# Performance work log

Hardware: AMD Instinct MI355X
Metric: run time of the kernel (lower is better)

## Reference

```python
import jax, jax.numpy as jnp
import numpy as np

B, S, D = 2, 1024, 4096
HQ, HKV, HD = 32, 8, 128
GROUPS = HQ // HKV          # 4
SCALE = HD ** -0.5


def _rope_tables(key):
    # standard RoPE cos/sin tables, non-interleaved (half-split) layout
    inv_freq = 1.0 / (10000.0 ** (jnp.arange(0, HD, 2, dtype=jnp.float32) / HD))  # [HD/2]
    pos = jnp.arange(S, dtype=jnp.float32)                                        # [S]
    freqs = pos[:, None] * inv_freq[None, :]                                      # [S, HD/2]
    emb = jnp.concatenate([freqs, freqs], axis=-1)                                # [S, HD]
    cos = jnp.broadcast_to(jnp.cos(emb)[None], (B, S, HD))
    sin = jnp.broadcast_to(jnp.sin(emb)[None], (B, S, HD))
    return cos, sin


def setup_inputs() -> dict:
    key = jax.random.key(0)
    ks = jax.random.split(key, 6)
    hidden_states = jax.random.normal(ks[0], (B, S, D), dtype=jnp.float32)
    cos_table, sin_table = _rope_tables(ks[1])
    Wq = jax.random.normal(ks[2], (D, HQ * HD), dtype=jnp.float32) * (D ** -0.5)
    Wk = jax.random.normal(ks[3], (D, HKV * HD), dtype=jnp.float32) * (D ** -0.5)
    Wv = jax.random.normal(ks[4], (D, HKV * HD), dtype=jnp.float32) * (D ** -0.5)
    Wo = jax.random.normal(ks[5], (HQ * HD, D), dtype=jnp.float32) * ((HQ * HD) ** -0.5)
    return {"hidden_states": hidden_states, "cos_table": cos_table,
            "sin_table": sin_table, "Wq": Wq, "Wk": Wk, "Wv": Wv, "Wo": Wo}


def _rotate_half(x):
    x1, x2 = jnp.split(x, 2, axis=-1)
    return jnp.concatenate([-x2, x1], axis=-1)


def _apply_rope(x, cos, sin):
    # x: [B, S, H, HD]; cos/sin: [B, S, HD] broadcast across heads
    c = cos[:, :, None, :]
    s = sin[:, :, None, :]
    return x * c + _rotate_half(x) * s


def reference(hidden_states, cos_table, sin_table, Wq, Wk, Wv, Wo):
    b, s, _ = hidden_states.shape
    # QKV projections (no bias, Llama-style)
    q = (hidden_states @ Wq).reshape(b, s, HQ, HD)
    k = (hidden_states @ Wk).reshape(b, s, HKV, HD)
    v = (hidden_states @ Wv).reshape(b, s, HKV, HD)
    # fused RoPE on q and k (in [B, S, H, HD] layout, as in source)
    q = _apply_rope(q, cos_table, sin_table)
    k = _apply_rope(k, cos_table, sin_table)
    # -> [B, H, S, HD]
    q = q.transpose(0, 2, 1, 3)
    k = k.transpose(0, 2, 1, 3)
    v = v.transpose(0, 2, 1, 3)
    # GQA repeat_kv: [B, HKV, S, HD] -> [B, HQ, S, HD]
    k = jnp.repeat(k, GROUPS, axis=1)
    v = jnp.repeat(v, GROUPS, axis=1)
    # SDPA, no mask (source calls sdpa without a mask)
    scores = jnp.einsum('bhqd,bhkd->bhqk', q, k) * SCALE
    attn = jax.nn.softmax(scores, axis=-1)
    out = jnp.einsum('bhqk,bhkd->bhqd', attn, v)
    out = out.transpose(0, 2, 1, 3).reshape(b, s, HQ * HD)
    return out @ Wo
```

## Files before the change

kernel.cpp:

```cpp
#include <hip/hip_runtime.h>

#define B_   2
#define S_   1024
#define D_   4096
#define HQ_  32
#define HKV_ 8
#define HD_  128
#define SCALE_ 0.08838834764831845f

typedef unsigned short u16;
typedef __attribute__((ext_vector_type(8))) short s16x8;
typedef __attribute__((ext_vector_type(4))) short s16x4;
typedef __attribute__((ext_vector_type(4))) float f32x4;

#define MFMA(a,b,c) __builtin_amdgcn_mfma_f32_16x16x32_bf16((a),(b),(c),0,0,0)

__device__ __forceinline__ u16 bf16_rne(float x) {
  unsigned u = __float_as_uint(x);
  u += 0x7fffu + ((u >> 16) & 1u);
  return (u16)(u >> 16);
}
__device__ __forceinline__ float bf16_up(u16 h) {
  return __uint_as_float(((unsigned)h) << 16);
}
__device__ __forceinline__ void split2(float x, u16& h, u16& l) {
  h = bf16_rne(x);
  l = bf16_rne(x - bf16_up(h));
}

__device__ __forceinline__ void cvt_hi_lo(float a, float b, unsigned& hi, unsigned& lo) {
  unsigned h, l;
  asm("v_cvt_pk_bf16_f32 %0, %1, %2" : "=v"(h) : "v"(a), "v"(b));
  float ra = __uint_as_float(h << 16);
  float rb = __uint_as_float(h & 0xffff0000u);
  float la = a - ra, lb = b - rb;
  asm("v_cvt_pk_bf16_f32 %0, %1, %2" : "=v"(l) : "v"(la), "v"(lb));
  hi = h; lo = l;
}
__device__ __forceinline__ void pack8(float4 x, float4 y, uint4& h, uint4& l) {
  unsigned h0,h1,h2,h3,l0,l1,l2,l3;
  cvt_hi_lo(x.x, x.y, h0, l0);
  cvt_hi_lo(x.z, x.w, h1, l1);
  cvt_hi_lo(y.x, y.y, h2, l2);
  cvt_hi_lo(y.z, y.w, h3, l3);
  h = make_uint4(h0,h1,h2,h3); l = make_uint4(l0,l1,l2,l3);
}

typedef const __attribute__((address_space(1))) void* gas_ptr;
typedef __attribute__((address_space(3))) void* las_ptr;
__device__ __forceinline__ void gload_lds16(const void* g, void* l) {
  __builtin_amdgcn_global_load_lds((gas_ptr)g, (las_ptr)l, 16, 0, 0);
}

__global__ __launch_bounds__(256) void frag_b2(
    const float* __restrict__ W, u16* __restrict__ dh, u16* __restrict__ dl,
    int N, int n0, int Ntot16, int ntoff)
{
  __shared__ float T[32][68];
  const int kt = blockIdx.x, nbk = blockIdx.y;
  const int tid = threadIdx.x;
#pragma unroll
  for (int rep = 0; rep < 2; ++rep) {
    int idx = tid + rep * 256;
    int row = idx >> 4, c4 = (idx & 15) * 4;
    float4 v = *reinterpret_cast<const float4*>(&W[(size_t)(kt*32 + row) * N + n0 + nbk*64 + c4]);
    *reinterpret_cast<float4*>(&T[row][c4]) = v;
  }
  __syncthreads();
  int c = tid;
  int nt = c >> 6, l = c & 63;
  const size_t base = (((size_t)(kt >> 1) * Ntot16 + ntoff + nbk*4 + nt) * 2 + (kt & 1)) * 512;
  u16 hh[8], ll[8];
#pragma unroll
  for (int j = 0; j < 8; ++j) split2(T[(l >> 4)*8 + j][nt*16 + (l & 15)], hh[j], ll[j]);
  *reinterpret_cast<s16x8*>(&dh[base + (size_t)l * 8]) =
    (s16x8){(short)hh[0],(short)hh[1],(short)hh[2],(short)hh[3],
            (short)hh[4],(short)hh[5],(short)hh[6],(short)hh[7]};
  *reinterpret_cast<s16x8*>(&dl[base + (size_t)l * 8]) =
    (s16x8){(short)ll[0],(short)ll[1],(short)ll[2],(short)ll[3],
            (short)ll[4],(short)ll[5],(short)ll[6],(short)ll[7]};
}

__global__ __launch_bounds__(256) void frag_a(
    const float* __restrict__ src, u16* __restrict__ dh, u16* __restrict__ dl)
{
  __shared__ float T[128][68];
  const int kt = blockIdx.x;
  const int mb = blockIdx.y;
  const int tid = threadIdx.x;
#pragma unroll
  for (int rep = 0; rep < 8; ++rep) {
    int idx = tid + rep * 256;
    int row = idx >> 4, c4 = (idx & 15) * 4;
    float4 v = *reinterpret_cast<const float4*>(&src[(size_t)(mb*128 + row) * 4096 + kt*64 + c4]);
    *reinterpret_cast<float4*>(&T[row][c4]) = v;
  }
  __syncthreads();
#pragma unroll
  for (int rep = 0; rep < 4; ++rep) {
    int c = tid + rep * 256;
    int mt = c >> 7, rem = c & 127, kk = rem >> 6, l = rem & 63;
    u16 hh[8], ll[8];
#pragma unroll
    for (int j = 0; j < 8; ++j)
      split2(T[mt*16 + (l & 15)][kk*32 + (l >> 4)*8 + j], hh[j], ll[j]);
    size_t off = (((size_t)(kt*128 + mb*8 + mt)) * 2 + kk) * 512 + (size_t)l * 8;
    *reinterpret_cast<s16x8*>(&dh[off]) =
      (s16x8){(short)hh[0],(short)hh[1],(short)hh[2],(short)hh[3],
              (short)hh[4],(short)hh[5],(short)hh[6],(short)hh[7]};
    *reinterpret_cast<s16x8*>(&dl[off]) =
      (s16x8){(short)ll[0],(short)ll[1],(short)ll[2],(short)ll[3],
              (short)ll[4],(short)ll[5],(short)ll[6],(short)ll[7]};
  }
}

template<int NF, bool RQ>
__device__ __forceinline__ void gemm256_core(
    const u16* __restrict__ PAh, const u16* __restrict__ PAl,
    const u16* __restrict__ PBh, const u16* __restrict__ PBl,
    float* __restrict__ C0, float* __restrict__ C1, float* __restrict__ C2,
    int ldc0, int Nt16, int mb, int nb, int k0, int nk, u16* L)
{
  const int tid  = threadIdx.x;
  const int lane = tid & 63;
  const int wid  = tid >> 6;
  const int loff = lane * 8;
  const int wm8  = (wid >> 2) * 8;
  const int wnf  = (wid & 3) * NF;

  u16* A0 = L;
  u16* A1 = L + 16384;
  u16* B0 = L + 32768;
  u16* B1 = L + 32768 + NF*4096;

  f32x4 acc[8][NF];
#pragma unroll
  for (int i = 0; i < 8; ++i)
#pragma unroll
    for (int j = 0; j < NF; ++j) acc[i][j] = (f32x4){0.f,0.f,0.f,0.f};

  auto STAGE = [&](int t, u16* la_, u16* lb_) {
    const int kt64 = t >> 1, kk = t & 1;
    const size_t aSlab = (size_t)kt64 * 131072;
    const size_t bSlab = (size_t)kt64 * ((size_t)Nt16 * 1024);
    const int NCH = 32 + 8*NF;
#pragma unroll
    for (int c = wid; c < NCH; c += 8) {
      const u16* src; u16* dst;
      if (c < 16) {
        src = PAh + aSlab + (((size_t)(mb*16 + c))*2 + kk)*512;
        dst = la_ + c*512;
      } else if (c < 32) {
        int m = c - 16;
        src = PAl + aSlab + (((size_t)(mb*16 + m))*2 + kk)*512;
        dst = la_ + 8192 + m*512;
      } else if (c < 32 + 4*NF) {
        int n = c - 32;
        src = PBh + bSlab + (((size_t)(nb*4*NF + n))*2 + kk)*512;
        dst = lb_ + n*512;
      } else {
        int n = c - 32 - 4*NF;
        src = PBl + bSlab + (((size_t)(nb*4*NF + n))*2 + kk)*512;
        dst = lb_ + NF*2048 + n*512;
      }
      gload_lds16(src + loff, dst);
    }
  };

  STAGE(k0, (k0 & 1) ? A1 : A0, (k0 & 1) ? B1 : B0);
  __syncthreads();

  for (int t = k0; t < k0 + nk; ++t) {
    u16* la = (t & 1) ? A1 : A0;
    u16* lb = (t & 1) ? B1 : B0;
    if (t + 1 < k0 + nk)
      STAGE(t + 1, (t & 1) ? A0 : A1, (t & 1) ? B0 : B1);

    s16x8 ah[8], al[8], bh[NF], bl[NF];
#pragma unroll
    for (int mf = 0; mf < 8; ++mf)
      ah[mf] = *reinterpret_cast<const s16x8*>(&la[(wm8+mf)*512 + loff]);
#pragma unroll
    for (int nf = 0; nf < NF; ++nf)
      bh[nf] = *reinterpret_cast<const s16x8*>(&lb[(wnf+nf)*512 + loff]);
    __builtin_amdgcn_s_setprio(1);
#pragma unroll
    for (int nf = 0; nf < NF; ++nf)
#pragma unroll
      for (int mf = 0; mf < 8; ++mf)
        acc[mf][nf] = MFMA(ah[mf], bh[nf], acc[mf][nf]);
    __builtin_amdgcn_s_setprio(0);
#pragma unroll
    for (int mf = 0; mf < 8; ++mf)
      al[mf] = *reinterpret_cast<const s16x8*>(&la[8192 + (wm8+mf)*512 + loff]);
    __builtin_amdgcn_s_setprio(1);
#pragma unroll
    for (int nf = 0; nf < NF; ++nf)
#pragma unroll
      for (int mf = 0; mf < 8; ++mf)
        acc[mf][nf] = MFMA(al[mf], bh[nf], acc[mf][nf]);
    __builtin_amdgcn_s_setprio(0);
#pragma unroll
    for (int nf = 0; nf < NF; ++nf)
      bl[nf] = *reinterpret_cast<const s16x8*>(&lb[NF*2048 + (wnf+nf)*512 + loff]);
    __builtin_amdgcn_s_setprio(1);
#pragma unroll
    for (int nf = 0; nf < NF; ++nf)
#pragma unroll
      for (int mf = 0; mf < 8; ++mf)
        acc[mf][nf] = MFMA(ah[mf], bl[nf], acc[mf][nf]);
    __builtin_amdgcn_s_setprio(0);
    __syncthreads();
  }

  const int lg = lane >> 4, lr = lane & 15;
  const int rowb = mb*256 + (wid >> 2) * 128;
#pragma unroll
  for (int mf = 0; mf < 8; ++mf)
#pragma unroll
    for (int nf = 0; nf < NF; ++nf)
#pragma unroll
      for (int r = 0; r < 4; ++r) {
        int row = rowb + mf*16 + lg*4 + r;
        float v = acc[mf][nf][r];
        if constexpr (RQ) {
          int gcol = nb*(NF*64) + (wid & 3)*(NF*16) + nf*16 + lr;
          if (gcol < 4096)      C0[(size_t)row * 4096 + gcol] = v;
          else if (gcol < 5120) C1[(size_t)row * 1024 + (gcol - 4096)] = v;
          else                  C2[(size_t)row * 1024 + (gcol - 5120)] = v;
        } else {
          int col = nb*(NF*64) + (wid & 3)*(NF*16) + nf*16 + lr;
          C0[(size_t)row * ldc0 + col] = v;
        }
      }
}

__global__ __launch_bounds__(512) void gemm_qkv3(
    const u16* __restrict__ XAh, const u16* __restrict__ XAl,
    const u16* __restrict__ WBh, const u16* __restrict__ WBl,
    float* __restrict__ qb, float* __restrict__ kb, float* __restrict__ vb)
{
  __shared__ __attribute__((aligned(16))) u16 L[57344];
  int id = blockIdx.x;
  int swz = (id & 7) * 32 + (id >> 3);
  int mb = swz >> 5, nb = swz & 31;
  gemm256_core<3, true>(XAh, XAl, WBh, WBl, qb, kb, vb, 0, 384, mb, nb, 0, 128, L);
}

__global__ __launch_bounds__(512) void gemm_qkv2(
    const u16* __restrict__ XAh, const u16* __restrict__ XAl,
    const u16* __restrict__ WA,
    float* __restrict__ qb, float* __restrict__ kb, float* __restrict__ vb)
{
  __shared__ __attribute__((aligned(16))) u16 L[65536];
  int id = blockIdx.x;
  int swz = (id & 7) * 24 + (id >> 3);
  const u16 *Bh, *Bl; float* C; int ldc, Nt16, mb, nb;
  if (swz < 128)      { Bh = WA;          Bl = WA+16777216; C = qb; ldc = 4096; Nt16 = 256; mb = swz & 7;  nb = swz >> 3; }
  else if (swz < 160) { int u = swz-128; Bh = WA+33554432; Bl = WA+37748736; C = kb; ldc = 1024; Nt16 = 64; mb = u & 7; nb = u >> 3; }
  else                { int u = swz-160; Bh = WA+41943040; Bl = WA+46137344; C = vb; ldc = 1024; Nt16 = 64; mb = u & 7; nb = u >> 3; }
  gemm256_core<4, false>(XAh, XAl, Bh, Bl, C, nullptr, nullptr, ldc, Nt16, mb, nb, 0, 128, L);
}

__global__ __launch_bounds__(512) void gemm_out2(
    const u16* __restrict__ ABh, const u16* __restrict__ ABl,
    const u16* __restrict__ WOh, const u16* __restrict__ WOl,
    float* __restrict__ outp, float* __restrict__ c2)
{
  __shared__ __attribute__((aligned(16))) u16 L[65536];
  int id = blockIdx.x;
  int swz = (id & 7) * 32 + (id >> 3);
  int u = swz & 127, s = swz >> 7;
  int mb = u & 7, nb = u >> 3;
  gemm256_core<4, false>(ABh, ABl, WOh, WOl, s ? c2 : outp, nullptr, nullptr,
                         4096, 256, mb, nb, s*64, 64, L);
}

__global__ __launch_bounds__(256) void add_out(
    float* __restrict__ o, const float* __restrict__ c2)
{
  int i = blockIdx.x * 256 + threadIdx.x;
  float4 a = reinterpret_cast<float4*>(o)[i];
  float4 b = reinterpret_cast<const float4*>(c2)[i];
  a.x += b.x; a.y += b.y; a.z += b.z; a.w += b.w;
  reinterpret_cast<float4*>(o)[i] = a;
}

__global__ __launch_bounds__(256) void frag_kv(
    const float* __restrict__ kb, const float* __restrict__ vb,
    const float* __restrict__ cosT, const float* __restrict__ sinT,
    u16* __restrict__ KFh, u16* __restrict__ KFl,
    u16* __restrict__ VFh, u16* __restrict__ VFl)
{
  __shared__ float T[32][132];
  const int bid  = blockIdx.x;
  const int isV  = bid >> 9;
  const int bkvh = (bid >> 5) & 15;
  const int chnk = bid & 31;
  const int tid  = threadIdx.x;
  const int b    = bkvh >> 3, kvh = bkvh & 7;

  const float* src = isV ? vb : kb;
  {
    int r0 = tid >> 5, c4 = (tid & 31) * 4;
    float sgn = (c4 < 64) ? -1.f : 1.f;
#pragma unroll
    for (int it = 0; it < 4; ++it) {
      int row = r0 + it * 8;
      int srow = chnk*32 + row;
      const float* rp = &src[(((size_t)(b * S_ + srow)) * HKV_ + kvh) * HD_];
      float4 v = *reinterpret_cast<const float4*>(rp + c4);
      if (!isV) {
        float4 p  = *reinterpret_cast<const float4*>(rp + (c4 ^ 64));
        float4 cc = *reinterpret_cast<const float4*>(&cosT[((size_t)(b*S_ + srow))*HD_ + c4]);
        float4 ss = *reinterpret_cast<const float4*>(&sinT[((size_t)(b*S_ + srow))*HD_ + c4]);
        v.x = v.x*cc.x + sgn*p.x*ss.x;
        v.y = v.y*cc.y + sgn*p.y*ss.y;
        v.z = v.z*cc.z + sgn*p.z*ss.z;
        v.w = v.w*cc.w + sgn*p.w*ss.w;
      }
      *reinterpret_cast<float4*>(&T[row][c4]) = v;
    }
  }
  __syncthreads();
#pragma unroll
  for (int rep = 0; rep < 2; ++rep) {
    int c2 = tid + rep * 256;
    int l = c2 & 63;
    u16 hh[8], ll[8];
    if (!isV) {
      int f = c2 >> 6, st_loc = f >> 2, dt = f & 3;
#pragma unroll
      for (int j = 0; j < 8; ++j)
        split2(T[st_loc*16 + (l & 15)][dt*32 + (l >> 4)*8 + j], hh[j], ll[j]);
      size_t off = ((size_t)bkvh*64 + chnk*2) * 2048 + (size_t)c2 * 8;
      *reinterpret_cast<s16x8*>(&KFh[off]) =
        (s16x8){(short)hh[0],(short)hh[1],(short)hh[2],(short)hh[3],
                (short)hh[4],(short)hh[5],(short)hh[6],(short)hh[7]};
      *reinterpret_cast<s16x8*>(&KFl[off]) =
        (s16x8){(short)ll[0],(short)ll[1],(short)ll[2],(short)ll[3],
                (short)ll[4],(short)ll[5],(short)ll[6],(short)ll[7]};
    } else {
      int dt16 = c2 >> 6;
#pragma unroll
      for (int j = 0; j < 8; ++j)
        split2(T[(l >> 4)*8 + j][dt16*16 + (l & 15)], hh[j], ll[j]);
      size_t off = ((size_t)bkvh*32 + chnk) * 4096 + (size_t)c2 * 8;
      *reinterpret_cast<s16x8*>(&VFh[off]) =
        (s16x8){(short)hh[0],(short)hh[1],(short)hh[2],(short)hh[3],
                (short)hh[4],(short)hh[5],(short)hh[6],(short)hh[7]};
      *reinterpret_cast<s16x8*>(&VFl[off]) =
        (s16x8){(short)ll[0],(short)ll[1],(short)ll[2],(short)ll[3],
                (short)ll[4],(short)ll[5],(short)ll[6],(short)ll[7]};
    }
  }
}

__global__ __launch_bounds__(512) void attn3(
    const float* __restrict__ qb,
    const float* __restrict__ cosT, const float* __restrict__ sinT,
    const u16* __restrict__ KFh, const u16* __restrict__ KFl,
    const u16* __restrict__ VFh, const u16* __restrict__ VFl,
    float* __restrict__ ob)
{
  __shared__ __attribute__((aligned(16))) u16 Klds[16384];
  __shared__ __attribute__((aligned(16))) u16 Vlds[16384];
  __shared__ u16 Ph[8][16][68], Pl[8][16][68];

  const int tid  = threadIdx.x;
  const int lane = tid & 63;
  const int wid  = tid >> 6;
  const int lr   = lane & 15;
  const int lg   = lane >> 4;
  const int loff = lane * 8;
  const int qt   = blockIdx.x;
  const int bh   = blockIdx.y;
  const int b    = bh >> 5, h = bh & 31;
  const int bkvh = b * 8 + (h >> 2);

  s16x8 qh[4], ql[4];
  {
    const int qrow = qt * 128 + wid * 16 + lr;
    const float* qp = qb + ((size_t)((b * S_ + qrow) * HQ_ + h)) * HD_;
    const float* cp = cosT + ((size_t)(b * S_ + qrow)) * HD_;
    const float* sp = sinT + ((size_t)(b * S_ + qrow)) * HD_;
#pragma unroll
    for (int kc = 0; kc < 4; ++kc) {
      const int d0 = kc * 32 + lg * 8;
      const float sgn = (d0 < 64) ? -1.f : 1.f;
      float4 v0 = *reinterpret_cast<const float4*>(qp + d0);
      float4 v1 = *reinterpret_cast<const float4*>(qp + d0 + 4);
      float4 p0 = *reinterpret_cast<const float4*>(qp + (d0 ^ 64));
      float4 p1 = *reinterpret_cast<const float4*>(qp + (d0 ^ 64) + 4);
      float4 c0 = *reinterpret_cast<const float4*>(cp + d0);
      float4 c1 = *reinterpret_cast<const float4*>(cp + d0 + 4);
      float4 s0 = *reinterpret_cast<const float4*>(sp + d0);
      float4 s1 = *reinterpret_cast<const float4*>(sp + d0 + 4);
      float4 r0, r1;
      r0.x = v0.x*c0.x + sgn*p0.x*s0.x;  r0.y = v0.y*c0.y + sgn*p0.y*s0.y;
      r0.z = v0.z*c0.z + sgn*p0.z*s0.z;  r0.w = v0.w*c0.w + sgn*p0.w*s0.w;
      r1.x = v1.x*c1.x + sgn*p1.x*s1.x;  r1.y = v1.y*c1.y + sgn*p1.y*s1.y;
      r1.z = v1.z*c1.z + sgn*p1.z*s1.z;  r1.w = v1.w*c1.w + sgn*p1.w*s1.w;
      uint4 h4, l4; pack8(r0, r1, h4, l4);
      qh[kc] = *reinterpret_cast<s16x8*>(&h4);
      ql[kc] = *reinterpret_cast<s16x8*>(&l4);
    }
  }

  f32x4 acc_o[8];
#pragma unroll
  for (int df = 0; df < 8; ++df) acc_o[df] = (f32x4){0.f, 0.f, 0.f, 0.f};
  float m_run[4] = {-1e30f, -1e30f, -1e30f, -1e30f};
  float l_run[4] = {0.f, 0.f, 0.f, 0.f};

  const u16* gKh = KFh + (size_t)bkvh * 131072;
  const u16* gKl = KFl + (size_t)bkvh * 131072;
  const u16* gVh = VFh + (size_t)bkvh * 131072;
  const u16* gVl = VFl + (size_t)bkvh * 131072;

#pragma unroll
  for (int i = 0; i < 4; ++i) {
    int idx = wid * 4 + i;
    const u16* src = (idx < 16) ? (gKh + idx*512) : (gKl + (idx-16)*512);
    u16* dst = Klds + ((idx < 16) ? idx*512 : 8192 + (idx-16)*512);
    gload_lds16(src + loff, dst);
  }
  __syncthreads();

  for (int t = 0; t < 16; ++t) {
#pragma unroll
    for (int i = 0; i < 4; ++i) {
      int idx = wid * 4 + i;
      const u16* src = (idx < 16) ? (gVh + t*8192 + idx*512)
                                  : (gVl + t*8192 + (idx-16)*512);
      u16* dst = Vlds + ((idx < 16) ? idx*512 : 8192 + (idx-16)*512);
      gload_lds16(src + loff, dst);
    }

    f32x4 accs[4];
#pragma unroll
    for (int nf = 0; nf < 4; ++nf) {
      accs[nf] = (f32x4){0.f, 0.f, 0.f, 0.f};
      s16x8 kh8[4], kl8[4];
#pragma unroll
      for (int kc = 0; kc < 4; ++kc) {
        kh8[kc] = *reinterpret_cast<const s16x8*>(&Klds[nf*2048 + kc*512 + loff]);
        kl8[kc] = *reinterpret_cast<const s16x8*>(&Klds[8192 + nf*2048 + kc*512 + loff]);
      }
#pragma unroll
      for (int kc = 0; kc < 4; ++kc) {
        accs[nf] = MFMA(qh[kc], kh8[kc], accs[nf]);
        accs[nf] = MFMA(ql[kc], kh8[kc], accs[nf]);
        accs[nf] = MFMA(qh[kc], kl8[kc], accs[nf]);
      }
    }
#pragma unroll
    for (int nf = 0; nf < 4; ++nf) accs[nf] *= SCALE_;

    float corr[4], rsum[4];
#pragma unroll
    for (int r = 0; r < 4; ++r) {
      float t0 = fmaxf(fmaxf(accs[0][r], accs[1][r]), fmaxf(accs[2][r], accs[3][r]));
      t0 = fmaxf(t0, __shfl_xor(t0, 1));
      t0 = fmaxf(t0, __shfl_xor(t0, 2));
      t0 = fmaxf(t0, __shfl_xor(t0, 4));
      t0 = fmaxf(t0, __shfl_xor(t0, 8));
      float mnew = fmaxf(m_run[r], t0);
      corr[r] = __expf(m_run[r] - mnew);
      m_run[r] = mnew;
      rsum[r] = 0.f;
    }
#pragma unroll
    for (int nf = 0; nf < 4; ++nf)
#pragma unroll
      for (int r = 0; r < 4; ++r) {
        float p = __expf(accs[nf][r] - m_run[r]);
        rsum[r] += p;
        u16 ph, pl;
        split2(p, ph, pl);
        Ph[wid][lg*4 + r][nf*16 + lr] = ph;
        Pl[wid][lg*4 + r][nf*16 + lr] = pl;
      }
#pragma unroll
    for (int r = 0; r < 4; ++r) {
      float s = rsum[r];
      s += __shfl_xor(s, 1); s += __shfl_xor(s, 2);
      s += __shfl_xor(s, 4); s += __shfl_xor(s, 8);
      l_run[r] = l_run[r] * corr[r] + s;
    }
#pragma unroll
    for (int df = 0; df < 8; ++df)
#pragma unroll
      for (int r = 0; r < 4; ++r) acc_o[df][r] *= corr[r];

    __syncthreads();

    if (t < 15) {
#pragma unroll
      for (int i = 0; i < 4; ++i) {
        int idx = wid * 4 + i;
        const u16* src = (idx < 16) ? (gKh + (t+1)*8192 + idx*512)
                                    : (gKl + (t+1)*8192 + (idx-16)*512);
        u16* dst = Klds + ((idx < 16) ? idx*512 : 8192 + (idx-16)*512);
        gload_lds16(src + loff, dst);
      }
    }

    s16x8 pa_h[2], pa_l[2];
#pragma unroll
    for (int kc = 0; kc < 2; ++kc) {
      pa_h[kc] = *reinterpret_cast<const s16x8*>(&Ph[wid][lr][kc*32 + lg*8]);
      pa_l[kc] = *reinterpret_cast<const s16x8*>(&Pl[wid][lr][kc*32 + lg*8]);
    }
#pragma unroll
    for (int df = 0; df < 8; ++df) {
      s16x8 vh8[2], vl8[2];
#pragma unroll
      for (int kc = 0; kc < 2; ++kc) {
        vh8[kc] = *reinterpret_cast<const s16x8*>(&Vlds[kc*4096 + df*512 + loff]);
        vl8[kc] = *reinterpret_cast<const s16x8*>(&Vlds[8192 + kc*4096 + df*512 + loff]);
      }
#pragma unroll
      for (int kc = 0; kc < 2; ++kc) {
        acc_o[df] = MFMA(pa_h[kc], vh8[kc], acc_o[df]);
        acc_o[df] = MFMA(pa_l[kc], vh8[kc], acc_o[df]);
        acc_o[df] = MFMA(pa_h[kc], vl8[kc], acc_o[df]);
      }
    }
    __syncthreads();
  }

  float inv_l[4];
#pragma unroll
  for (int r = 0; r < 4; ++r) inv_l[r] = 1.f / l_run[r];
#pragma unroll
  for (int df = 0; df < 8; ++df)
#pragma unroll
    for (int r = 0; r < 4; ++r) {
      int row = qt * 128 + wid * 16 + lg * 4 + r;
      ob[((size_t)((b * S_ + row) * HQ_ + h)) * HD_ + df*16 + lr] = acc_o[df][r] * inv_l[r];
    }
}

extern "C" void kernel_launch(void* const* d_in, const int* in_sizes, int n_in,
                              void* d_out, int out_size, void* d_ws, size_t ws_size,
                              hipStream_t stream)
{
  const float* hs   = (const float*)d_in[0];
  const float* cosT = (const float*)d_in[1];
  const float* sinT = (const float*)d_in[2];
  const float* Wq   = (const float*)d_in[3];
  const float* Wk   = (const float*)d_in[4];
  const float* Wv   = (const float*)d_in[5];
  const float* Wo   = (const float*)d_in[6];
  float* out = (float*)d_out;

  float* qb = (float*)d_ws;
  float* kb = qb + 8388608;
  float* vb = kb + 2097152;
  float* ab = vb + 2097152;
  u16*   FR = (u16*)(ab + 8388608);

  const size_t WS212 = 222298112ULL;
  const size_t WS208 = 218103808ULL;

  if (ws_size >= WS212) {
    u16* XAh = FR;
    u16* XAl = FR + 8388608;
    u16* WBh = FR + 16777216;
    u16* WBl = FR + 41943040;
    u16* KFh = FR + 16777216;
    u16* KFl = FR + 18874368;
    u16* VFh = FR + 20971520;
    u16* VFl = FR + 23068672;
    u16* WOh = FR + 25165824;
    u16* WOl = FR + 41943040;

    frag_a<<<dim3(64,16), 256, 0, stream>>>(hs, XAh, XAl);
    frag_b2<<<dim3(128,64), 256, 0, stream>>>(Wq, WBh, WBl, 4096, 0, 384, 0);
    frag_b2<<<dim3(128,16), 256, 0, stream>>>(Wk, WBh, WBl, 1024, 0, 384, 256);
    frag_b2<<<dim3(128,16), 256, 0, stream>>>(Wv, WBh, WBl, 1024, 0, 384, 320);
    gemm_qkv3<<<256, 512, 0, stream>>>(XAh, XAl, WBh, WBl, qb, kb, vb);
    frag_kv<<<1024, 256, 0, stream>>>(kb, vb, cosT, sinT, KFh, KFl, VFh, VFl);
    frag_b2<<<dim3(128,64), 256, 0, stream>>>(Wo, WOh, WOl, 4096, 0, 256, 0);
    attn3<<<dim3(8, 64), 512, 0, stream>>>(qb, cosT, sinT, KFh, KFl, VFh, VFl, ab);
    frag_a<<<dim3(64,16), 256, 0, stream>>>(ab, XAh, XAl);
    gemm_out2<<<256, 512, 0, stream>>>(XAh, XAl, WOh, WOl, out, qb);
    add_out<<<8192, 256, 0, stream>>>(out, qb);
  } else {
    u16* XAh = FR;
    u16* XAl = FR + 8388608;
    u16* WA  = FR + 16777216;
    frag_a<<<dim3(64,16), 256, 0, stream>>>(hs, XAh, XAl);
    frag_b2<<<dim3(128,64), 256, 0, stream>>>(Wq, WA,           WA+16777216, 4096, 0, 256, 0);
    frag_b2<<<dim3(128,16), 256, 0, stream>>>(Wk, WA+33554432,  WA+37748736, 1024, 0, 64, 0);
    frag_b2<<<dim3(128,16), 256, 0, stream>>>(Wv, WA+41943040,  WA+46137344, 1024, 0, 64, 0);
    gemm_qkv2<<<192, 512, 0, stream>>>(XAh, XAl, WA, qb, kb, vb);
    frag_kv<<<1024, 256, 0, stream>>>(kb, vb, cosT, sinT,
                                      WA, WA+2097152, WA+4194304, WA+6291456);
    frag_b2<<<dim3(128,64), 256, 0, stream>>>(Wo, WA+8388608, WA+25165824, 4096, 0, 256, 0);
    attn3<<<dim3(8, 64), 512, 0, stream>>>(qb, cosT, sinT,
                                           WA, WA+2097152, WA+4194304, WA+6291456, ab);
    frag_a<<<dim3(64,16), 256, 0, stream>>>(ab, XAh, XAl);
    gemm_out2<<<256, 512, 0, stream>>>(XAh, XAl, WA+8388608, WA+25165824, out, qb);
    add_out<<<8192, 256, 0, stream>>>(out, qb);
  }
}
```

Baseline: 642.7 us.

## Use 128-row GEMM tiles for QKV and out-proj, drop split-K reduction

Adds a gemm128_core with a 128-row M tile and full-K double-buffered LDS staging. The QKV GEMM now launches 512 smaller blocks instead of 256, and the output projection becomes one full-K kernel writing directly to out, replacing the split-K gemm_out2 plus add_out. This aims to improve CU occupancy and wave balance and to remove the extra partial-sum buffer traffic and the reduction kernel. In exchange, each block reuses loaded data less and the B operand is read from memory more often.

```diff
diff --git a/kernel.cpp b/kernel.cpp
--- a/kernel.cpp
+++ b/kernel.cpp
@@ -112,6 +112,152 @@
       (s16x8){(short)ll[0],(short)ll[1],(short)ll[2],(short)ll[3],
               (short)ll[4],(short)ll[5],(short)ll[6],(short)ll[7]};
   }
+}
+
+template<int NF, bool RQ>
+__device__ __forceinline__ void gemm128_core(
+    const u16* __restrict__ PAh, const u16* __restrict__ PAl,
+    const u16* __restrict__ PBh, const u16* __restrict__ PBl,
+    float* __restrict__ C0, float* __restrict__ C1, float* __restrict__ C2,
+    int ldc0, int Nt16, int mb, int nb, u16* L)
+{
+  const int tid  = threadIdx.x;
+  const int lane = tid & 63;
+  const int wid  = tid >> 6;
+  const int loff = lane * 8;
+  const int wm4  = (wid >> 2) * 4;
+  const int wnf  = (wid & 3) * NF;
+  const int BNT  = 4 * NF;
+
+  u16* A0 = L;
+  u16* A1 = L + 8192;
+  u16* B0 = L + 16384;
+  u16* B1 = L + 16384 + BNT*1024;
+
+  f32x4 acc[4][NF];
+#pragma unroll
+  for (int i = 0; i < 4; ++i)
+#pragma unroll
+    for (int j = 0; j < NF; ++j) acc[i][j] = (f32x4){0.f,0.f,0.f,0.f};
+
+  auto STAGE = [&](int t, u16* la_, u16* lb_) {
+    const int kt64 = t >> 1, kk = t & 1;
+    const size_t aSlab = (size_t)kt64 * 131072;
+    const size_t bSlab = (size_t)kt64 * ((size_t)Nt16 * 1024);
+    const int NCH = 16 + 2*BNT;
+#pragma unroll
+    for (int c = wid; c < NCH; c += 8) {
+      const u16* src; u16* dst;
+      if (c < 8) {
+        src = PAh + aSlab + (((size_t)(mb*8 + c))*2 + kk)*512;
+        dst = la_ + c*512;
+      } else if (c < 16) {
+        int m = c - 8;
+        src = PAl + aSlab + (((size_t)(mb*8 + m))*2 + kk)*512;
+        dst = la_ + 4096 + m*512;
+      } else if (c < 16 + BNT) {
+        int n = c - 16;
+        src = PBh + bSlab + (((size_t)(nb*BNT + n))*2 + kk)*512;
+        dst = lb_ + n*512;
+      } else {
+        int n = c - 16 - BNT;
+        src = PBl + bSlab + (((size_t)(nb*BNT + n))*2 + kk)*512;
+        dst = lb_ + BNT*512 + n*512;
+      }
+      gload_lds16(src + loff, dst);
+    }
+  };
+
+  STAGE(0, A0, B0);
+  __syncthreads();
+
+  for (int t = 0; t < 128; ++t) {
+    u16* la = (t & 1) ? A1 : A0;
+    u16* lb = (t & 1) ? B1 : B0;
+    if (t < 127)
+      STAGE(t + 1, (t & 1) ? A0 : A1, (t & 1) ? B0 : B1);
+
+    s16x8 ah[4], al[4], bh[NF], bl[NF];
+#pragma unroll
+    for (int mf = 0; mf < 4; ++mf)
+      ah[mf] = *reinterpret_cast<const s16x8*>(&la[(wm4+mf)*512 + loff]);
+#pragma unroll
+    for (int nf = 0; nf < NF; ++nf)
+      bh[nf] = *reinterpret_cast<const s16x8*>(&lb[(wnf+nf)*512 + loff]);
+    __builtin_amdgcn_s_setprio(1);
+#pragma unroll
+    for (int nf = 0; nf < NF; ++nf)
+#pragma unroll
+      for (int mf = 0; mf < 4; ++mf)
+        acc[mf][nf] = MFMA(ah[mf], bh[nf], acc[mf][nf]);
+    __builtin_amdgcn_s_setprio(0);
+#pragma unroll
+    for (int mf = 0; mf < 4; ++mf)
+      al[mf] = *reinterpret_cast<const s16x8*>(&la[4096 + (wm4+mf)*512 + loff]);
+    __builtin_amdgcn_s_setprio(1);
+#pragma unroll
+    for (int nf = 0; nf < NF; ++nf)
+#pragma unroll
+      for (int mf = 0; mf < 4; ++mf)
+        acc[mf][nf] = MFMA(al[mf], bh[nf], acc[mf][nf]);
+    __builtin_amdgcn_s_setprio(0);
+#pragma unroll
+    for (int nf = 0; nf < NF; ++nf)
+      bl[nf] = *reinterpret_cast<const s16x8*>(&lb[BNT*512 + (wnf+nf)*512 + loff]);
+    __builtin_amdgcn_s_setprio(1);
+#pragma unroll
+    for (int nf = 0; nf < NF; ++nf)
+#pragma unroll
+      for (int mf = 0; mf < 4; ++mf)
+        acc[mf][nf] = MFMA(ah[mf], bl[nf], acc[mf][nf]);
+    __builtin_amdgcn_s_setprio(0);
+    __syncthreads();
+  }
+
+  const int lg = lane >> 4, lr = lane & 15;
+  const int rowb = mb*128 + (wid >> 2) * 64;
+#pragma unroll
+  for (int mf = 0; mf < 4; ++mf)
+#pragma unroll
+    for (int nf = 0; nf < NF; ++nf)
+#pragma unroll
+      for (int r = 0; r < 4; ++r) {
+        int row = rowb + mf*16 + lg*4 + r;
+        float v = acc[mf][nf][r];
+        int gcol = nb*(NF*64) + (wid & 3)*(NF*16) + nf*16 + lr;
+        if constexpr (RQ) {
+          if (gcol < 4096)      C0[(size_t)row * 4096 + gcol] = v;
+          else if (gcol < 5120) C1[(size_t)row * 1024 + (gcol - 4096)] = v;
+          else                  C2[(size_t)row * 1024 + (gcol - 5120)] = v;
+        } else {
+          C0[(size_t)row * ldc0 + gcol] = v;
+        }
+      }
+}
+
+__global__ __launch_bounds__(512, 4) void gemm_qkv3(
+    const u16* __restrict__ XAh, const u16* __restrict__ XAl,
+    const u16* __restrict__ WBh, const u16* __restrict__ WBl,
+    float* __restrict__ qb, float* __restrict__ kb, float* __restrict__ vb)
+{
+  __shared__ __attribute__((aligned(16))) u16 L[40960];
+  int id = blockIdx.x;
+  int swz = (id & 7) * 64 + (id >> 3);
+  int mb = swz >> 5, nb = swz & 31;
+  gemm128_core<3, true>(XAh, XAl, WBh, WBl, qb, kb, vb, 0, 384, mb, nb, L);
+}
+
+__global__ __launch_bounds__(512, 4) void gemm_out3(
+    const u16* __restrict__ ABh, const u16* __restrict__ ABl,
+    const u16* __restrict__ WOh, const u16* __restrict__ WOl,
+    float* __restrict__ outp)
+{
+  __shared__ __attribute__((aligned(16))) u16 L[32768];
+  int id = blockIdx.x;
+  int swz = (id & 7) * 64 + (id >> 3);
+  int mb = swz >> 5, nb = swz & 31;
+  gemm128_core<2, false>(ABh, ABl, WOh, WOl, outp, nullptr, nullptr,
+                         4096, 256, mb, nb, L);
 }
 
 template<int NF, bool RQ>
@@ -233,18 +379,6 @@
           C0[(size_t)row * ldc0 + col] = v;
         }
       }
-}
-
-__global__ __launch_bounds__(512) void gemm_qkv3(
-    const u16* __restrict__ XAh, const u16* __restrict__ XAl,
-    const u16* __restrict__ WBh, const u16* __restrict__ WBl,
-    float* __restrict__ qb, float* __restrict__ kb, float* __restrict__ vb)
-{
-  __shared__ __attribute__((aligned(16))) u16 L[57344];
-  int id = blockIdx.x;
-  int swz = (id & 7) * 32 + (id >> 3);
-  int mb = swz >> 5, nb = swz & 31;
-  gemm256_core<3, true>(XAh, XAl, WBh, WBl, qb, kb, vb, 0, 384, mb, nb, 0, 128, L);
 }
 
 __global__ __launch_bounds__(512) void gemm_qkv2(
@@ -562,7 +696,6 @@
   u16*   FR = (u16*)(ab + 8388608);
 
   const size_t WS212 = 222298112ULL;
-  const size_t WS208 = 218103808ULL;
 
   if (ws_size >= WS212) {
     u16* XAh = FR;
@@ -580,13 +713,12 @@
     frag_b2<<<dim3(128,64), 256, 0, stream>>>(Wq, WBh, WBl, 4096, 0, 384, 0);
     frag_b2<<<dim3(128,16), 256, 0, stream>>>(Wk, WBh, WBl, 1024, 0, 384, 256);
     frag_b2<<<dim3(128,16), 256, 0, stream>>>(Wv, WBh, WBl, 1024, 0, 384, 320);
-    gemm_qkv3<<<256, 512, 0, stream>>>(XAh, XAl, WBh, WBl, qb, kb, vb);
+    gemm_qkv3<<<512, 512, 0, stream>>>(XAh, XAl, WBh, WBl, qb, kb, vb);
     frag_kv<<<1024, 256, 0, stream>>>(kb, vb, cosT, sinT, KFh, KFl, VFh, VFl);
     frag_b2<<<dim3(128,64), 256, 0, stream>>>(Wo, WOh, WOl, 4096, 0, 256, 0);
     attn3<<<dim3(8, 64), 512, 0, stream>>>(qb, cosT, sinT, KFh, KFl, VFh, VFl, ab);
     frag_a<<<dim3(64,16), 256, 0, stream>>>(ab, XAh, XAl);
-    gemm_out2<<<256, 512, 0, stream>>>(XAh, XAl, WOh, WOl, out, qb);
-    add_out<<<8192, 256, 0, stream>>>(out, qb);
+    gemm_out3<<<512, 512, 0, stream>>>(XAh, XAl, WOh, WOl, out);
   } else {
     u16* XAh = FR;
     u16* XAl = FR + 8388608;
```

Result: slower. 691.0 us (+7.5%).
